# Kernel tuning notes

Hardware: AMD Instinct MI355X
Metric: run time of the kernel (lower is better)

Reference implementation:

```python
import jax, jax.numpy as jnp
import numpy as np

B, K, D = 4096, 100, 64          # batch, multi_factor*top_k, emb_dim
NU, NI = 100000, 50000           # n_users, n_items
MLP_DIMS = [2 * K, K, K // 2, 25, 12, 1]  # 200,100,50,25,12,1


def setup_inputs() -> dict:
    key = jax.random.key(0)
    ks = jax.random.split(key, 30)
    inp = {
        "user_idxs": jax.random.randint(ks[0], (B,), 0, NU),
        "item_idxs": jax.random.randint(ks[1], (B,), 0, NI),
        "user_idx_tensor": jax.random.randint(ks[2], (NU, K), 0, NU),
        "item_idx_tensor": jax.random.randint(ks[3], (NI, K), 0, NI),
        "user_scr_tensor": jax.random.uniform(ks[4], (NU, K), dtype=jnp.float32),
        "item_scr_tensor": jax.random.uniform(ks[5], (NI, K), dtype=jnp.float32),
        "user_emb": jax.random.normal(ks[6], (NU, D), dtype=jnp.float32),
        "item_emb": jax.random.normal(ks[7], (NI, D), dtype=jnp.float32),
    }
    i = 8
    for net in ("n1", "n2"):
        for li, (a, b) in enumerate(zip(MLP_DIMS[:-1], MLP_DIMS[1:]), 1):
            lim = 1.0 / np.sqrt(a)
            inp[f"{net}_w{li}"] = jax.random.uniform(ks[i], (a, b), minval=-lim, maxval=lim, dtype=jnp.float32); i += 1
            inp[f"{net}_b{li}"] = jax.random.uniform(ks[i], (b,), minval=-lim, maxval=lim, dtype=jnp.float32); i += 1
    return inp


def _mlp(x, ws, bs):
    for w, b in zip(ws[:-1], bs[:-1]):
        x = jax.nn.relu(x @ w + b)
    return x @ ws[-1] + bs[-1]


def reference(user_idxs, item_idxs, user_idx_tensor, item_idx_tensor,
              user_scr_tensor, item_scr_tensor, user_emb, item_emb,
              n1_w1, n1_b1, n1_w2, n1_b2, n1_w3, n1_b3, n1_w4, n1_b4, n1_w5, n1_b5,
              n2_w1, n2_b1, n2_w2, n2_b2, n2_w3, n2_b3, n2_w4, n2_b4, n2_w5, n2_b5):
    # neighbor gather: [B,K,D] embeddings and [B,K] scores
    u_e = user_emb[user_idx_tensor[user_idxs]]
    u_s = user_scr_tensor[user_idxs]
    i_e = item_emb[item_idx_tensor[item_idxs]]
    i_s = item_scr_tensor[item_idxs]
    # torch bmm(emb [B,K,D], score[:,None,:].repeat(1,D,1) [B,D,K]) -> [B,K,K];
    # since the repeated score matrix has identical rows, result = emb.sum(-1) (x) score
    su = u_e.sum(-1)[:, :, None] * u_s[:, None, :]  # [B,K,K]
    si = i_e.sum(-1)[:, :, None] * i_s[:, None, :]  # [B,K,K]
    # cat(dim=1).permute(0,2,1) == cat of transposes along last dim
    x1 = jnp.concatenate([su.transpose(0, 2, 1), si.transpose(0, 2, 1)], axis=2)  # [B,K,2K]
    x2 = jnp.concatenate([su, si], axis=2)                                        # [B,K,2K]
    ws1 = [n1_w1, n1_w2, n1_w3, n1_w4, n1_w5]; bs1 = [n1_b1, n1_b2, n1_b3, n1_b4, n1_b5]
    ws2 = [n2_w1, n2_w2, n2_w3, n2_w4, n2_w5]; bs2 = [n2_b1, n2_b2, n2_b3, n2_b4, n2_b5]
    c1 = _mlp(x1, ws1, bs1)[..., 0]  # [B,K]
    c2 = _mlp(x2, ws2, bs2)[..., 0]  # [B,K]
    return jax.nn.sigmoid(jnp.mean(c1 + c2, axis=1))  # [B]
```

## Files before the change

kernel.cpp:

```cpp
#include <hip/hip_runtime.h>
#include <math.h>

#define KDIM 100
#define DDIM 64

typedef __bf16 bf16x8 __attribute__((ext_vector_type(8)));
typedef float  f32x4  __attribute__((ext_vector_type(4)));
typedef float  f32x2  __attribute__((ext_vector_type(2)));
typedef unsigned int u32;
typedef u32 u32x2 __attribute__((ext_vector_type(2)));

struct Weights {
  const float *w1, *b1, *w2, *b2, *w3, *b3, *w4, *b4, *w5, *b5;
};

__device__ __forceinline__ f32x2 vmax2(f32x2 a, f32x2 b) {
#if __has_builtin(__builtin_elementwise_max)
  return __builtin_elementwise_max(a, b);
#else
  return (f32x2){fmaxf(a[0], b[0]), fmaxf(a[1], b[1])};
#endif
}

constexpr int L_VEC  = 0;
constexpr int L_PA   = 400;
constexpr int L_TAIL = 912;
constexpr int L_C    = 1424;
constexpr int SM_F   = 1680;
constexpr int H2T_BYTE = SM_F * 4;
constexpr int H3T_BYTE = H2T_BYTE + 8 * 2048;
constexpr int SM_BYTES = H3T_BYTE + 8 * 1024;

__global__ void prep_kernel(const float* __restrict__ user_emb,
                            const float* __restrict__ item_emb,
                            float* __restrict__ u_rowsum,
                            float* __restrict__ i_rowsum,
                            int NU, int NI, Weights N1, Weights N2,
                            __bf16* __restrict__ wfrag, float* __restrict__ tail) {
  const int tid  = threadIdx.x;
  const int lane = tid & 63;
  const int g = lane >> 4, c16 = lane & 15;
  const int gw = (blockIdx.x * blockDim.x + tid) >> 6;

  if (gw < 42) {
    const int net = gw / 21, f = gw % 21;
    const Weights W = net ? N2 : N1;
    bf16x8 v;
    if (f < 16) {
      const int mt = f >> 2, ks = f & 3;
      #pragma unroll
      for (int i = 0; i < 8; ++i) {
        const int k = 32 * ks + 8 * g + i, m = 16 * mt + c16;
        v[i] = (__bf16)((k < 100 && m < 50) ? W.w2[k * 50 + m] : 0.f);
      }
    } else if (f < 20) {
      const int mt = (f - 16) >> 1, ks = (f - 16) & 1;
      #pragma unroll
      for (int i = 0; i < 8; ++i) {
        const int k = 32 * ks + 8 * g + i, m = 16 * mt + c16;
        v[i] = (__bf16)((k < 50 && m < 25) ? W.w3[k * 25 + m] : 0.f);
      }
    } else {
      #pragma unroll
      for (int i = 0; i < 8; ++i) {
        const int k = 8 * g + i, m = c16;
        v[i] = (__bf16)((k < 25 && m < 12) ? W.w4[k * 12 + m] : 0.f);
      }
    }
    *(bf16x8*)(wfrag + (size_t)gw * 512 + lane * 8) = v;
  }

  if (blockIdx.x == 0) {
    for (int e = tid; e < 512; e += 256) {
      float v;
      if (e < 256)      { const int j = e & 127; const Weights W = (e & 128) ? N2 : N1; v = (j < 100) ? W.b1[j] : 0.f; }
      else if (e < 384) { const int t = e - 256; const int j = t & 63; const Weights W = (t & 64) ? N2 : N1; v = (j < 50) ? W.b2[j] : 0.f; }
      else if (e < 448) { const int t = e - 384; const int j = t & 31; const Weights W = (t & 32) ? N2 : N1; v = (j < 25) ? W.b3[j] : 0.f; }
      else if (e < 480) { const int t = e - 448; const int j = t & 15; const Weights W = (t & 16) ? N2 : N1; v = (j < 12) ? W.b4[j] : 0.f; }
      else              { const int t = e - 480; const int j = t & 15; const Weights W = (t & 16) ? N2 : N1; v = (j < 12) ? W.w5[j] : 0.f; }
      tail[e] = v;
    }
  }

  const int NR = NU + NI;
  const int chunk = lane & 15, lrow = lane >> 4;
  const int nwave = (gridDim.x * blockDim.x) >> 6;
  for (int base = gw * 4; base < NR; base += nwave * 4) {
    const int r = base + lrow;
    float s = 0.f;
    if (r < NR) {
      const float* src = (r < NU) ? (user_emb + (size_t)r * DDIM)
                                  : (item_emb + (size_t)(r - NU) * DDIM);
      const float4 v4 = ((const float4*)src)[chunk];
      s = v4.x + v4.y + v4.z + v4.w;
    }
    s += __shfl_xor(s, 1); s += __shfl_xor(s, 2);
    s += __shfl_xor(s, 4); s += __shfl_xor(s, 8);
    if (chunk == 0 && r < NR) {
      if (r < NU) u_rowsum[r] = s; else i_rowsum[r - NU] = s;
    }
  }
}

__global__ void __launch_bounds__(256) proj_kernel(
    const int* __restrict__ user_idxs, const int* __restrict__ item_idxs,
    const int* __restrict__ uidx_t, const int* __restrict__ iidx_t,
    const float* __restrict__ uscr, const float* __restrict__ iscr,
    const float* __restrict__ u_rowsum, const float* __restrict__ i_rowsum,
    const float* __restrict__ n1w1, const float* __restrict__ n2w1,
    float* __restrict__ VG, float* __restrict__ PAG, int B)
{
  __shared__ float VT[100][20];
  __shared__ float W1S[50][128];
  __shared__ int sidx[16];
  const int tid = threadIdx.x;
  const int sel = blockIdx.x & 3;
  const int b0  = (blockIdx.x >> 2) * 16;

  if (tid < 16) {
    const int b = b0 + tid;
    const int bb = (b < B) ? b : (B - 1);
    sidx[tid] = (sel & 1) ? item_idxs[bb] : user_idxs[bb];
  }
  __syncthreads();

  {
    const int bl = tid >> 4, strip = tid & 15;
    const size_t row = (size_t)sidx[bl] * KDIM;
    if (sel < 2) {
      const int* it = (sel == 0) ? uidx_t : iidx_t;
      const float* rs = (sel == 0) ? u_rowsum : i_rowsum;
      int idxs[7];
      #pragma unroll
      for (int i = 0; i < 7; ++i) {
        const int k = strip + 16 * i;
        idxs[i] = (k < KDIM) ? it[row + k] : 0;
      }
      #pragma unroll
      for (int i = 0; i < 7; ++i) {
        const int k = strip + 16 * i;
        if (k < KDIM) VT[k][bl] = rs[idxs[i]];
      }
    } else {
      const float* sc = (sel == 2) ? uscr : iscr;
      #pragma unroll
      for (int i = 0; i < 7; ++i) {
        const int k = strip + 16 * i;
        if (k < KDIM) VT[k][bl] = sc[row + k];
      }
    }
  }

  const float* w1 = (sel < 2) ? n1w1 : n2w1;
  const int rb = (sel & 1) * KDIM;
  const int jg = tid & 31, bg = tid >> 5;
  float acc[2][4];
  #pragma unroll
  for (int bi = 0; bi < 2; ++bi)
    #pragma unroll
    for (int ji = 0; ji < 4; ++ji) acc[bi][ji] = 0.f;

  for (int kh = 0; kh < 2; ++kh) {
    __syncthreads();
    for (int e = tid; e < 1600; e += 256) {
      const int k = e >> 5, s = e & 31;
      float4 v;
      if (s < 25) v = ((const float4*)(w1 + (size_t)(rb + kh * 50 + k) * KDIM))[s];
      else        v = make_float4(0.f, 0.f, 0.f, 0.f);
      *(float4*)&W1S[k][4 * s] = v;
    }
    __syncthreads();
    #pragma unroll 2
    for (int k = 0; k < 50; ++k) {
      const f32x2 v = *(const f32x2*)&VT[kh * 50 + k][2 * bg];
      const float4 w = *(const float4*)&W1S[k][4 * jg];
      const float ww[4] = {w.x, w.y, w.z, w.w};
      #pragma unroll
      for (int ji = 0; ji < 4; ++ji) {
        acc[0][ji] = fmaf(v[0], ww[ji], acc[0][ji]);
        acc[1][ji] = fmaf(v[1], ww[ji], acc[1][ji]);
      }
    }
  }

  #pragma unroll
  for (int bi = 0; bi < 2; ++bi) {
    const int b = b0 + 2 * bg + bi;
    if (b < B) {
      float4 o = make_float4(acc[bi][0], acc[bi][1], acc[bi][2], acc[bi][3]);
      *(float4*)(PAG + ((size_t)sel * B + b) * 128 + 4 * jg) = o;
    }
  }
  {
    const int bl = tid >> 4, strip = tid & 15;
    const int b = b0 + bl;
    if (b < B) {
      float* dst = VG + ((size_t)sel * B + b) * KDIM;
      #pragma unroll
      for (int i = 0; i < 7; ++i) {
        const int k = strip + 16 * i;
        if (k < KDIM) dst[k] = VT[k][bl];
      }
    }
  }
}

__global__ void __launch_bounds__(256, 3) mlp_kernel(
    const float* __restrict__ VG, const float* __restrict__ PAG,
    const float* __restrict__ tail,
    const float* __restrict__ n1b5, const float* __restrict__ n2b5,
    const __bf16* __restrict__ wfrag, float* __restrict__ out, int B)
{
  __shared__ __align__(16) char smem[SM_BYTES];
  float* sm = (float*)smem;
  const int tid  = threadIdx.x;
  const int lane = tid & 63;
  const int wv   = tid >> 6;
  const int g    = lane >> 4;
  const int c16  = lane & 15;
  const int b    = blockIdx.x;
  const f32x2 Z2 = {0.f, 0.f};

  if (tid < 128) {
    const int sel = tid >> 5, s = tid & 31;
    *(float4*)&sm[L_PA + sel * 128 + 4 * s] =
        *(const float4*)(PAG + ((size_t)sel * B + b) * 128 + 4 * s);
  } else {
    const int t = tid - 128;
    *(float4*)&sm[L_TAIL + 4 * t] = *(const float4*)(tail + 4 * t);
  }
  if (tid < 200) {
    const int sel = tid / 50, r = tid % 50;
    *(f32x2*)&sm[L_VEC + sel * 100 + 2 * r] =
        *(const f32x2*)(VG + ((size_t)sel * B + b) * KDIM + 2 * r);
  }
  __syncthreads();

  const int net = wv >> 1;
  const int qp  = wv & 1;
  const int vA  = net ? (L_VEC + 0)   : (L_VEC + 200);
  const int vB  = net ? (L_VEC + 100) : (L_VEC + 300);
  const int pAo = L_PA + net * 256;
  const int pBo = pAo + 128;
  const char* wfb = (const char*)wfrag + net * 21 * 1024;
  char* h2t0 = smem + H2T_BYTE + (wv * 2 + 0) * 2048;
  char* h2t1 = smem + H2T_BYTE + (wv * 2 + 1) * 2048;
  char* h3t0 = smem + H3T_BYTE + (wv * 2 + 0) * 1024;
  char* h3t1 = smem + H3T_BYTE + (wv * 2 + 1) * 1024;
  const float b5v = net ? n2b5[0] : n1b5[0];
  const int t7 = c16 & 7, t3 = c16 & 3;

  float sAr[2][2], sBr[2][2];
  #pragma unroll
  for (int qt = 0; qt < 2; ++qt)
    #pragma unroll
    for (int c = 0; c < 2; ++c) {
      const int row = 25 * (2 * qp + qt) + 16 * c + c16;
      const int rr = row < KDIM ? row : (KDIM - 1);
      sAr[qt][c] = sm[vA + rr]; sBr[qt][c] = sm[vB + rr];
    }

  f32x4 acc2[2][2][4];
  #pragma unroll
  for (int qt = 0; qt < 2; ++qt)
    #pragma unroll
    for (int c = 0; c < 2; ++c)
      #pragma unroll
      for (int mt = 0; mt < 4; ++mt) acc2[qt][c][mt] = (f32x4){0.f, 0.f, 0.f, 0.f};

  #pragma unroll
  for (int ks = 0; ks < 4; ++ks) {
    const int jb = 32 * ks + 8 * g;
    const f32x2* pa2 = (const f32x2*)&sm[pAo + jb];
    const f32x2* pb2 = (const f32x2*)&sm[pBo + jb];
    const f32x2* b12 = (const f32x2*)&sm[L_TAIL + net * 128 + jb];
    f32x2 paf[4], pbf[4], b1f[4];
    #pragma unroll
    for (int i = 0; i < 4; ++i) { paf[i] = pa2[i]; pbf[i] = pb2[i]; b1f[i] = b12[i]; }
    bf16x8 hb[2][2];
    #pragma unroll
    for (int qt = 0; qt < 2; ++qt)
      #pragma unroll
      for (int c = 0; c < 2; ++c) {
        const f32x2 sa = {sAr[qt][c], sAr[qt][c]}, sb = {sBr[qt][c], sBr[qt][c]};
        bf16x8 a;
        #pragma unroll
        for (int i2 = 0; i2 < 4; ++i2) {
          f32x2 t = sb * pbf[i2] + b1f[i2];
          t = sa * paf[i2] + t;
          t = vmax2(t, Z2);
          a[2 * i2]     = (__bf16)t[0];
          a[2 * i2 + 1] = (__bf16)t[1];
        }
        hb[qt][c] = a;
      }
    __builtin_amdgcn_s_setprio(1);
    #pragma unroll
    for (int mt = 0; mt < 4; ++mt) {
      const bf16x8 a = *(const bf16x8*)(wfb + (mt * 4 + ks) * 1024 + lane * 16);
      #pragma unroll
      for (int qt = 0; qt < 2; ++qt) {
        acc2[qt][0][mt] = __builtin_amdgcn_mfma_f32_16x16x32_bf16(a, hb[qt][0], acc2[qt][0][mt], 0, 0, 0);
        acc2[qt][1][mt] = __builtin_amdgcn_mfma_f32_16x16x32_bf16(a, hb[qt][1], acc2[qt][1][mt], 0, 0, 0);
      }
    }
    __builtin_amdgcn_s_setprio(0);
  }

  #pragma unroll
  for (int c = 0; c < 2; ++c) {
    #pragma unroll
    for (int qt = 0; qt < 2; ++qt) {
      char* h2t = qt ? h2t1 : h2t0;
      #pragma unroll
      for (int mt = 0; mt < 4; ++mt) {
        const f32x2* b2p = (const f32x2*)&sm[L_TAIL + 256 + net * 64 + 16 * mt + 4 * g];
        const f32x4 x = acc2[qt][c][mt];
        const f32x2 lo = vmax2((f32x2){x[0], x[1]} + b2p[0], Z2);
        const f32x2 hi = vmax2((f32x2){x[2], x[3]} + b2p[1], Z2);
        union { __bf16 e[4]; u32x2 w; } o;
        o.e[0] = (__bf16)lo[0]; o.e[1] = (__bf16)lo[1];
        o.e[2] = (__bf16)hi[0]; o.e[3] = (__bf16)hi[1];
        const int S = (2 * mt + (g >> 1)) ^ t7;
        *(u32x2*)(h2t + c16 * 128 + S * 16 + (g & 1) * 8) = o.w;
      }
    }

    f32x4 acc3[2][2];
    #pragma unroll
    for (int qt = 0; qt < 2; ++qt)
      #pragma unroll
      for (int mt = 0; mt < 2; ++mt) acc3[qt][mt] = (f32x4){0.f, 0.f, 0.f, 0.f};
    #pragma unroll
    for (int ks = 0; ks < 2; ++ks) {
      const int S = (4 * ks + g) ^ t7;
      const bf16x8 hbf0 = *(const bf16x8*)(h2t0 + c16 * 128 + S * 16);
      const bf16x8 hbf1 = *(const bf16x8*)(h2t1 + c16 * 128 + S * 16);
      __builtin_amdgcn_s_setprio(1);
      #pragma unroll
      for (int mt = 0; mt < 2; ++mt) {
        const bf16x8 a = *(const bf16x8*)(wfb + (16 + mt * 2 + ks) * 1024 + lane * 16);
        acc3[0][mt] = __builtin_amdgcn_mfma_f32_16x16x32_bf16(a, hbf0, acc3[0][mt], 0, 0, 0);
        acc3[1][mt] = __builtin_amdgcn_mfma_f32_16x16x32_bf16(a, hbf1, acc3[1][mt], 0, 0, 0);
      }
      __builtin_amdgcn_s_setprio(0);
    }
    #pragma unroll
    for (int qt = 0; qt < 2; ++qt) {
      char* h3t = qt ? h3t1 : h3t0;
      #pragma unroll
      for (int mt = 0; mt < 2; ++mt) {
        const f32x2* b3p = (const f32x2*)&sm[L_TAIL + 384 + net * 32 + 16 * mt + 4 * g];
        const f32x4 x = acc3[qt][mt];
        const f32x2 lo = vmax2((f32x2){x[0], x[1]} + b3p[0], Z2);
        const f32x2 hi = vmax2((f32x2){x[2], x[3]} + b3p[1], Z2);
        union { __bf16 e[4]; u32x2 w; } o;
        o.e[0] = (__bf16)lo[0]; o.e[1] = (__bf16)lo[1];
        o.e[2] = (__bf16)hi[0]; o.e[3] = (__bf16)hi[1];
        const int S = (2 * mt + (g >> 1)) ^ t3;
        *(u32x2*)(h3t + c16 * 64 + S * 16 + (g & 1) * 8) = o.w;
      }
    }

    {
      const int S = g ^ t3;
      const bf16x8 hbf0 = *(const bf16x8*)(h3t0 + c16 * 64 + S * 16);
      const bf16x8 hbf1 = *(const bf16x8*)(h3t1 + c16 * 64 + S * 16);
      const bf16x8 a = *(const bf16x8*)(wfb + 20 * 1024 + lane * 16);
      const f32x4 z = {0.f, 0.f, 0.f, 0.f};
      __builtin_amdgcn_s_setprio(1);
      const f32x4 acc4_0 = __builtin_amdgcn_mfma_f32_16x16x32_bf16(a, hbf0, z, 0, 0, 0);
      const f32x4 acc4_1 = __builtin_amdgcn_mfma_f32_16x16x32_bf16(a, hbf1, z, 0, 0, 0);
      __builtin_amdgcn_s_setprio(0);
      const f32x2* b4p = (const f32x2*)&sm[L_TAIL + 448 + net * 16 + 4 * g];
      const f32x2* w5p = (const f32x2*)&sm[L_TAIL + 480 + net * 16 + 4 * g];
      #pragma unroll
      for (int qt = 0; qt < 2; ++qt) {
        const f32x4 x = qt ? acc4_1 : acc4_0;
        const f32x2 lo = vmax2((f32x2){x[0], x[1]} + b4p[0], Z2);
        const f32x2 hi = vmax2((f32x2){x[2], x[3]} + b4p[1], Z2);
        float v = lo[0] * w5p[0][0] + lo[1] * w5p[0][1]
                + hi[0] * w5p[1][0] + hi[1] * w5p[1][1];
        v += __shfl_xor(v, 16); v += __shfl_xor(v, 32);
        const int lr = 16 * c + c16;
        if (g == 0 && lr < 25)
          sm[L_C + net * 128 + 25 * (2 * qp + qt) + lr] = v + b5v;
      }
    }
  }
  __syncthreads();

  float v = 0.f;
  if (tid < KDIM) v = sm[L_C + tid] + sm[L_C + 128 + tid];
  if (tid < 128) {
    #pragma unroll
    for (int d = 1; d < 64; d <<= 1) v += __shfl_xor(v, d);
    if ((tid & 63) == 0) sm[tid >> 6] = v;
  }
  __syncthreads();
  if (tid == 0) out[b] = 1.f / (1.f + expf(-0.01f * (sm[0] + sm[1])));
}

extern "C" void kernel_launch(void* const* d_in, const int* in_sizes, int n_in,
                              void* d_out, int out_size, void* d_ws, size_t ws_size,
                              hipStream_t stream) {
  const int*   user_idxs = (const int*)d_in[0];
  const int*   item_idxs = (const int*)d_in[1];
  const int*   uidx_t    = (const int*)d_in[2];
  const int*   iidx_t    = (const int*)d_in[3];
  const float* uscr      = (const float*)d_in[4];
  const float* iscr      = (const float*)d_in[5];
  const float* uemb      = (const float*)d_in[6];
  const float* iemb      = (const float*)d_in[7];

  const int B  = in_sizes[0];
  const int NU = in_sizes[6] / DDIM;
  const int NI = in_sizes[7] / DDIM;

  Weights N1 { (const float*)d_in[8],  (const float*)d_in[9],
               (const float*)d_in[10], (const float*)d_in[11],
               (const float*)d_in[12], (const float*)d_in[13],
               (const float*)d_in[14], (const float*)d_in[15],
               (const float*)d_in[16], (const float*)d_in[17] };
  Weights N2 { (const float*)d_in[18], (const float*)d_in[19],
               (const float*)d_in[20], (const float*)d_in[21],
               (const float*)d_in[22], (const float*)d_in[23],
               (const float*)d_in[24], (const float*)d_in[25],
               (const float*)d_in[26], (const float*)d_in[27] };

  char* ws = (char*)d_ws;
  float* u_rowsum = (float*)ws;
  float* i_rowsum = u_rowsum + NU;
  size_t off = (((size_t)(NU + NI) * 4 + 1023) & ~(size_t)1023);
  __bf16* wfrag = (__bf16*)(ws + off);
  float*  tail  = (float*)(wfrag + (size_t)42 * 512);
  off += (((size_t)42 * 512 * 2 + 512 * 4 + 1023) & ~(size_t)1023);
  float* VG  = (float*)(ws + off);
  off += (size_t)4 * B * KDIM * 4;
  float* PAG = (float*)(ws + off);

  float* out = (float*)d_out;

  prep_kernel<<<1024, 256, 0, stream>>>(uemb, iemb, u_rowsum, i_rowsum, NU, NI, N1, N2, wfrag, tail);
  const int nbt = (B + 15) / 16;
  proj_kernel<<<nbt * 4, 256, 0, stream>>>(user_idxs, item_idxs, uidx_t, iidx_t,
                                           uscr, iscr, u_rowsum, i_rowsum,
                                           N1.w1, N2.w1, VG, PAG, B);
  mlp_kernel<<<B, 256, 0, stream>>>(VG, PAG, tail, N1.b5, N2.b5, wfrag, out, B);
}
```

Before: 76.18 us.

## Compute first-layer projection with bf16 MFMA using prepacked W1 fragments

The scalar FP32 FMA projection in proj_kernel, which reloads W1 into shared memory twice per block, is replaced by bf16 MFMA 16x16x32 instructions. W1 fragments are prepacked in prep_kernel into a workspace buffer. The shared-memory layout switches to batch-major with padding, and the separate index-load sync is removed. This cuts per-block W1 staging and ALU work, at the cost of bf16 precision in the first-layer projection.

```diff
diff --git a/kernel.cpp b/kernel.cpp
--- a/kernel.cpp
+++ b/kernel.cpp
@@ -36,7 +36,8 @@
                             float* __restrict__ u_rowsum,
                             float* __restrict__ i_rowsum,
                             int NU, int NI, Weights N1, Weights N2,
-                            __bf16* __restrict__ wfrag, float* __restrict__ tail) {
+                            __bf16* __restrict__ wfrag, float* __restrict__ tail,
+                            __bf16* __restrict__ w1frag) {
   const int tid  = threadIdx.x;
   const int lane = tid & 63;
   const int g = lane >> 4, c16 = lane & 15;
@@ -68,6 +69,20 @@
       }
     }
     *(bf16x8*)(wfrag + (size_t)gw * 512 + lane * 8) = v;
+  } else if (gw < 170) {
+    const int t = gw - 42;
+    const int sel = t >> 5;
+    const int f = t & 31;
+    const int mt = f >> 2, ks = f & 3;
+    const float* w1 = (sel < 2) ? N1.w1 : N2.w1;
+    const int rb = (sel & 1) * KDIM;
+    bf16x8 v;
+    #pragma unroll
+    for (int i = 0; i < 8; ++i) {
+      const int k = 32 * ks + 8 * g + i, n = 16 * mt + c16;
+      v[i] = (__bf16)((k < KDIM && n < KDIM) ? w1[(size_t)(rb + k) * KDIM + n] : 0.f);
+    }
+    *(bf16x8*)(w1frag + (size_t)t * 512 + lane * 8) = v;
   }
 
   if (blockIdx.x == 0) {
@@ -107,90 +122,51 @@
     const int* __restrict__ uidx_t, const int* __restrict__ iidx_t,
     const float* __restrict__ uscr, const float* __restrict__ iscr,
     const float* __restrict__ u_rowsum, const float* __restrict__ i_rowsum,
-    const float* __restrict__ n1w1, const float* __restrict__ n2w1,
+    const __bf16* __restrict__ w1frag,
     float* __restrict__ VG, float* __restrict__ PAG, int B)
 {
-  __shared__ float VT[100][20];
-  __shared__ float W1S[50][128];
-  __shared__ int sidx[16];
+  __shared__ float VT[16][132];
   const int tid = threadIdx.x;
+  const int lane = tid & 63;
+  const int wv  = tid >> 6;
+  const int g = lane >> 4, c16 = lane & 15;
   const int sel = blockIdx.x & 3;
   const int b0  = (blockIdx.x >> 2) * 16;
 
-  if (tid < 16) {
-    const int b = b0 + tid;
-    const int bb = (b < B) ? b : (B - 1);
-    sidx[tid] = (sel & 1) ? item_idxs[bb] : user_idxs[bb];
-  }
-  __syncthreads();
-
   {
     const int bl = tid >> 4, strip = tid & 15;
-    const size_t row = (size_t)sidx[bl] * KDIM;
-    if (sel < 2) {
-      const int* it = (sel == 0) ? uidx_t : iidx_t;
-      const float* rs = (sel == 0) ? u_rowsum : i_rowsum;
-      int idxs[7];
-      #pragma unroll
-      for (int i = 0; i < 7; ++i) {
+    const int b = b0 + bl;
+    const int bb = (b < B) ? b : (B - 1);
+    const int sb = (sel & 1) ? item_idxs[bb] : user_idxs[bb];
+    const size_t row = (size_t)sb * KDIM;
+    if (sel == 0) {
+      #pragma unroll
+      for (int i = 0; i < 8; ++i) {
         const int k = strip + 16 * i;
-        idxs[i] = (k < KDIM) ? it[row + k] : 0;
-      }
-      #pragma unroll
-      for (int i = 0; i < 7; ++i) {
+        VT[bl][k] = (k < KDIM) ? u_rowsum[uidx_t[row + k]] : 0.f;
+      }
+    } else if (sel == 1) {
+      #pragma unroll
+      for (int i = 0; i < 8; ++i) {
         const int k = strip + 16 * i;
-        if (k < KDIM) VT[k][bl] = rs[idxs[i]];
+        VT[bl][k] = (k < KDIM) ? i_rowsum[iidx_t[row + k]] : 0.f;
+      }
+    } else if (sel == 2) {
+      #pragma unroll
+      for (int i = 0; i < 8; ++i) {
+        const int k = strip + 16 * i;
+        VT[bl][k] = (k < KDIM) ? uscr[row + k] : 0.f;
       }
     } else {
-      const float* sc = (sel == 2) ? uscr : iscr;
-      #pragma unroll
-      for (int i = 0; i < 7; ++i) {
+      #pragma unroll
+      for (int i = 0; i < 8; ++i) {
         const int k = strip + 16 * i;
-        if (k < KDIM) VT[k][bl] = sc[row + k];
-      }
-    }
-  }
-
-  const float* w1 = (sel < 2) ? n1w1 : n2w1;
-  const int rb = (sel & 1) * KDIM;
-  const int jg = tid & 31, bg = tid >> 5;
-  float acc[2][4];
-  #pragma unroll
-  for (int bi = 0; bi < 2; ++bi)
-    #pragma unroll
-    for (int ji = 0; ji < 4; ++ji) acc[bi][ji] = 0.f;
-
-  for (int kh = 0; kh < 2; ++kh) {
-    __syncthreads();
-    for (int e = tid; e < 1600; e += 256) {
-      const int k = e >> 5, s = e & 31;
-      float4 v;
-      if (s < 25) v = ((const float4*)(w1 + (size_t)(rb + kh * 50 + k) * KDIM))[s];
-      else        v = make_float4(0.f, 0.f, 0.f, 0.f);
-      *(float4*)&W1S[k][4 * s] = v;
-    }
-    __syncthreads();
-    #pragma unroll 2
-    for (int k = 0; k < 50; ++k) {
-      const f32x2 v = *(const f32x2*)&VT[kh * 50 + k][2 * bg];
-      const float4 w = *(const float4*)&W1S[k][4 * jg];
-      const float ww[4] = {w.x, w.y, w.z, w.w};
-      #pragma unroll
-      for (int ji = 0; ji < 4; ++ji) {
-        acc[0][ji] = fmaf(v[0], ww[ji], acc[0][ji]);
-        acc[1][ji] = fmaf(v[1], ww[ji], acc[1][ji]);
-      }
-    }
-  }
-
-  #pragma unroll
-  for (int bi = 0; bi < 2; ++bi) {
-    const int b = b0 + 2 * bg + bi;
-    if (b < B) {
-      float4 o = make_float4(acc[bi][0], acc[bi][1], acc[bi][2], acc[bi][3]);
-      *(float4*)(PAG + ((size_t)sel * B + b) * 128 + 4 * jg) = o;
-    }
-  }
+        VT[bl][k] = (k < KDIM) ? iscr[row + k] : 0.f;
+      }
+    }
+  }
+  __syncthreads();
+
   {
     const int bl = tid >> 4, strip = tid & 15;
     const int b = b0 + bl;
@@ -199,7 +175,41 @@
       #pragma unroll
       for (int i = 0; i < 7; ++i) {
         const int k = strip + 16 * i;
-        if (k < KDIM) dst[k] = VT[k][bl];
+        if (k < KDIM) dst[k] = VT[bl][k];
+      }
+    }
+  }
+
+  bf16x8 bf[4];
+  #pragma unroll
+  for (int ks = 0; ks < 4; ++ks) {
+    const float* src = &VT[c16][32 * ks + 8 * g];
+    bf16x8 a;
+    #pragma unroll
+    for (int i = 0; i < 8; ++i) a[i] = (__bf16)src[i];
+    bf[ks] = a;
+  }
+
+  f32x4 acc[2];
+  #pragma unroll
+  for (int m2 = 0; m2 < 2; ++m2) acc[m2] = (f32x4){0.f, 0.f, 0.f, 0.f};
+  #pragma unroll
+  for (int m2 = 0; m2 < 2; ++m2) {
+    const int mt = 2 * wv + m2;
+    #pragma unroll
+    for (int ks = 0; ks < 4; ++ks) {
+      const bf16x8 a = *(const bf16x8*)(w1frag + ((size_t)(sel * 32 + mt * 4 + ks)) * 512 + lane * 8);
+      acc[m2] = __builtin_amdgcn_mfma_f32_16x16x32_bf16(a, bf[ks], acc[m2], 0, 0, 0);
+    }
+  }
+
+  {
+    const int b = b0 + c16;
+    if (b < B) {
+      #pragma unroll
+      for (int m2 = 0; m2 < 2; ++m2) {
+        const int mt = 2 * wv + m2;
+        *(f32x4*)(PAG + ((size_t)sel * B + b) * 128 + 16 * mt + 4 * g) = acc[m2];
       }
     }
   }
@@ -434,17 +444,18 @@
   size_t off = (((size_t)(NU + NI) * 4 + 1023) & ~(size_t)1023);
   __bf16* wfrag = (__bf16*)(ws + off);
   float*  tail  = (float*)(wfrag + (size_t)42 * 512);
-  off += (((size_t)42 * 512 * 2 + 512 * 4 + 1023) & ~(size_t)1023);
+  __bf16* w1frag = (__bf16*)((char*)tail + 2048);
+  off += (((size_t)42 * 512 * 2 + 2048 + 131072 + 1023) & ~(size_t)1023);
   float* VG  = (float*)(ws + off);
   off += (size_t)4 * B * KDIM * 4;
   float* PAG = (float*)(ws + off);
 
   float* out = (float*)d_out;
 
-  prep_kernel<<<1024, 256, 0, stream>>>(uemb, iemb, u_rowsum, i_rowsum, NU, NI, N1, N2, wfrag, tail);
+  prep_kernel<<<1024, 256, 0, stream>>>(uemb, iemb, u_rowsum, i_rowsum, NU, NI, N1, N2, wfrag, tail, w1frag);
   const int nbt = (B + 15) / 16;
   proj_kernel<<<nbt * 4, 256, 0, stream>>>(user_idxs, item_idxs, uidx_t, iidx_t,
                                            uscr, iscr, u_rowsum, i_rowsum,
-                                           N1.w1, N2.w1, VG, PAG, B);
+                                           w1frag, VG, PAG, B);
   mlp_kernel<<<B, 256, 0, stream>>>(VG, PAG, tail, N1.b5, N2.b5, wfrag, out, B);
 }
```

New measurement: 68.95 us. 9.5% less time.
